# Performance work log

Measured on AMD Instinct MI355X. Metric: run time of the kernel, lower is better.

Reference implementation:

```python
import jax, jax.numpy as jnp
import numpy as np

B, N, M, D = 256, 256, 256, 4
BIG = 1e10  # stand-in for +inf that keeps grads of unselected branches finite


def chamfer_split(target, reco, in_pid, out_pid):
    # masks of 'real' (non-zero pid) particles
    mask_x = in_pid != 0          # [B, N]
    mask_y = out_pid != 0         # [B, M]
    nx = jnp.sum(mask_x, axis=-1)  # [B] actual counts
    ny = jnp.sum(mask_y, axis=-1)
    n_in = jnp.maximum(1, nx).astype(target.dtype)   # max(1, n_in_part)
    n_out = jnp.maximum(1, ny).astype(target.dtype)  # max(1, n_out_part)

    # pairwise euclidean distances [B, N, M]
    diff = target[:, :, None, :] - reco[:, None, :, :]   # [B, N, M, D]
    dist = jnp.sqrt(jnp.sum(diff * diff, axis=-1))       # [B, N, M]

    # masked dual-axis mins (invalid entries pushed to BIG)
    min_xy = jnp.min(jnp.where(mask_y[:, None, :], dist, BIG), axis=-1)  # [B, N]
    min_yx = jnp.min(jnp.where(mask_x[:, :, None], dist, BIG), axis=-2)  # [B, M]
    sum_xy = jnp.sum(jnp.where(mask_x, min_xy, 0.0), axis=-1)  # [B]
    sum_yx = jnp.sum(jnp.where(mask_y, min_yx, 0.0), axis=-1)  # [B]

    normal = 0.5 * (sum_xy / n_out + sum_yx / n_in)  # [B]

    # edge cases: no reco non-zero particles -> sum||x_nz|| / max(1,nx);
    # no target non-zero particles -> sum over empty set = 0
    norm_x = jnp.linalg.norm(target, axis=-1)                    # [B, N]
    sum_norm_x_nz = jnp.sum(jnp.where(mask_x, norm_x, 0.0), -1)  # [B]
    eucl_non_zero = jnp.where(ny == 0, sum_norm_x_nz / n_in,
                              jnp.where(nx == 0, jnp.zeros_like(normal), normal))

    # zero-pid reco particles: mean L2 norm over zero entries
    norm_y = jnp.linalg.norm(reco, axis=-1)                          # [B, M]
    sum_norm_y_zero = jnp.sum(jnp.where(~mask_y, norm_y, 0.0), -1)   # [B]
    n_zero = jnp.maximum(1, reco.shape[1] - ny).astype(reco.dtype)
    eucl_zero = sum_norm_y_zero / n_zero

    # reduction == 'mean'
    return jnp.mean(eucl_non_zero), jnp.mean(eucl_zero)


def setup_inputs() -> dict:
    key = jax.random.key(0)
    k1, k2, k3, k4 = jax.random.split(key, 4)
    target = jax.random.normal(k1, (B, N, D), dtype=jnp.float32)
    reco = jax.random.normal(k2, (B, M, D), dtype=jnp.float32)
    in_pid = jax.random.randint(k3, (B, N), 0, 5, dtype=jnp.int32)
    out_pid = jax.random.randint(k4, (B, M), 0, 5, dtype=jnp.int32)
    return {"target": target, "reco": reco, "in_pid": in_pid, "out_pid": out_pid}


def reference(target, reco, in_pid, out_pid):
    return chamfer_split(target, reco, in_pid, out_pid)
```

## Files before the change

kernel.cpp:

```cpp
#include <hip/hip_runtime.h>
#include <math.h>

#define BB 256
#define NN 256
#define MM 256

#define POISON  1.0e18f
#define MINSENT 3.0e38f

__global__ __launch_bounds__(1024) void chamfer_split_kernel(
    const float* __restrict__ target,
    const float* __restrict__ reco,
    const int*   __restrict__ in_pid,
    const int*   __restrict__ out_pid,
    float* __restrict__ out)
{
    const int b = blockIdx.x;
    const int t = threadIdx.x;

    __shared__ float4 sT[NN];
    __shared__ float4 sR[MM];
    __shared__ float  pmin1[4][NN];
    __shared__ float  pmin2[4][MM];
    __shared__ int    sNx, sNy;
    __shared__ float  wsum[4][4];

    float4 x = {0.f, 0.f, 0.f, 0.f};
    float4 y = {0.f, 0.f, 0.f, 0.f};
    int mx = 0, my = 0;
    if (t == 0) { sNx = 0; sNy = 0; }
    if (t < NN) {
        const float4* tg = (const float4*)(target + (size_t)b * NN * 4);
        const float4* rc = (const float4*)(reco   + (size_t)b * MM * 4);
        x = tg[t];
        y = rc[t];
        mx = (in_pid[b * NN + t] != 0);
        my = (out_pid[b * MM + t] != 0);
        float4 px = x, py = y;
        if (!mx) px = make_float4(POISON, POISON, POISON, POISON);
        if (!my) py = make_float4(POISON, POISON, POISON, POISON);
        sT[t] = px;
        sR[t] = py;
        unsigned long long bx = __ballot(mx);
        unsigned long long by = __ballot(my);
        if ((t & 63) == 0) {
            atomicAdd(&sNx, (int)__popcll(bx));
            atomicAdd(&sNy, (int)__popcll(by));
        }
    }
    __syncthreads();

    if (t < 512) {
        const int c  = t >> 7;
        const int n0 = t & 127;
        const float4 xa = sT[n0];
        const float4 xb = sT[n0 + 128];
        float ma = MINSENT, mb = MINSENT;
        const int mbase = c << 6;
        #pragma unroll 16
        for (int i = 0; i < 64; ++i) {
            const float4 r = sR[mbase + i];
            float d0 = xa.x - r.x, d1 = xa.y - r.y, d2 = xa.z - r.z, d3 = xa.w - r.w;
            float sa = fmaf(d0, d0, fmaf(d1, d1, fmaf(d2, d2, d3 * d3)));
            ma = fminf(ma, sa);
            d0 = xb.x - r.x; d1 = xb.y - r.y; d2 = xb.z - r.z; d3 = xb.w - r.w;
            float sb = fmaf(d0, d0, fmaf(d1, d1, fmaf(d2, d2, d3 * d3)));
            mb = fminf(mb, sb);
        }
        pmin1[c][n0]       = ma;
        pmin1[c][n0 + 128] = mb;
    } else {
        const int u  = t - 512;
        const int c  = u >> 7;
        const int m0 = u & 127;
        const float4 ya = sR[m0];
        const float4 yb = sR[m0 + 128];
        float ma = MINSENT, mb = MINSENT;
        const int nbase = c << 6;
        #pragma unroll 16
        for (int i = 0; i < 64; ++i) {
            const float4 p = sT[nbase + i];
            float d0 = p.x - ya.x, d1 = p.y - ya.y, d2 = p.z - ya.z, d3 = p.w - ya.w;
            float sa = fmaf(d0, d0, fmaf(d1, d1, fmaf(d2, d2, d3 * d3)));
            ma = fminf(ma, sa);
            d0 = p.x - yb.x; d1 = p.y - yb.y; d2 = p.z - yb.z; d3 = p.w - yb.w;
            float sb = fmaf(d0, d0, fmaf(d1, d1, fmaf(d2, d2, d3 * d3)));
            mb = fminf(mb, sb);
        }
        pmin2[c][m0]       = ma;
        pmin2[c][m0 + 128] = mb;
    }
    __syncthreads();

    float v_xy = 0.f, v_yx = 0.f, v_nx = 0.f, v_ny0 = 0.f;
    if (t < NN) {
        const float mxy = fminf(fminf(pmin1[0][t], pmin1[1][t]),
                                fminf(pmin1[2][t], pmin1[3][t]));
        const float myx = fminf(fminf(pmin2[0][t], pmin2[1][t]),
                                fminf(pmin2[2][t], pmin2[3][t]));
        v_xy = mx ? sqrtf(mxy) : 0.f;
        v_yx = my ? sqrtf(myx) : 0.f;
        const float normx = sqrtf(fmaf(x.x, x.x, fmaf(x.y, x.y, fmaf(x.z, x.z, x.w * x.w))));
        const float normy = sqrtf(fmaf(y.x, y.x, fmaf(y.y, y.y, fmaf(y.z, y.z, y.w * y.w))));
        v_nx  = mx ? normx : 0.f;
        v_ny0 = my ? 0.f : normy;

        #pragma unroll
        for (int off = 32; off > 0; off >>= 1) {
            v_xy  += __shfl_down(v_xy,  off, 64);
            v_yx  += __shfl_down(v_yx,  off, 64);
            v_nx  += __shfl_down(v_nx,  off, 64);
            v_ny0 += __shfl_down(v_ny0, off, 64);
        }
        if ((t & 63) == 0) {
            const int wave = t >> 6;
            wsum[wave][0] = v_xy;
            wsum[wave][1] = v_yx;
            wsum[wave][2] = v_nx;
            wsum[wave][3] = v_ny0;
        }
    }
    __syncthreads();

    if (t == 0) {
        float s_xy = 0.f, s_yx = 0.f, s_nx = 0.f, s_ny0 = 0.f;
        #pragma unroll
        for (int w = 0; w < 4; ++w) {
            s_xy  += wsum[w][0];
            s_yx  += wsum[w][1];
            s_nx  += wsum[w][2];
            s_ny0 += wsum[w][3];
        }
        const int   nx    = sNx;
        const int   ny    = sNy;
        const float n_in  = (float)max(1, nx);
        const float n_out = (float)max(1, ny);
        const float normal = 0.5f * (s_xy / n_out + s_yx / n_in);
        const float eucl_nz = (ny == 0) ? (s_nx / n_in)
                                        : ((nx == 0) ? 0.0f : normal);
        const float n_zero = (float)max(1, MM - ny);
        const float eucl_z = s_ny0 / n_zero;
        atomicAdd(&out[0], eucl_nz * (1.0f / BB));
        atomicAdd(&out[1], eucl_z  * (1.0f / BB));
    }
}

extern "C" void kernel_launch(void* const* d_in, const int* in_sizes, int n_in,
                              void* d_out, int out_size, void* d_ws, size_t ws_size,
                              hipStream_t stream) {
    const float* target  = (const float*)d_in[0];
    const float* reco    = (const float*)d_in[1];
    const int*   in_pid  = (const int*)d_in[2];
    const int*   out_pid = (const int*)d_in[3];
    float* out = (float*)d_out;

    hipMemsetAsync(out, 0, (size_t)out_size * sizeof(float), stream);

    chamfer_split_kernel<<<dim3(BB), dim3(1024), 0, stream>>>(
        target, reco, in_pid, out_pid, out);
}
```

Baseline: 74.61 us.

## Register-block 8 points per thread and replace atomics with a two-stage reduction

Each thread now keeps 8 own-side points in registers and scans a 16-element chunk of the other side. Every shared-memory load of the other point is therefore reused 8 times instead of 2, cutting LDS traffic per distance. The partial-min buffers grow to 16 chunks, which adds LDS footprint and a longer final min. The global atomics and the memset are replaced by a per-batch workspace write plus a small second kernel, trading one memset launch for one extra kernel launch with a deterministic sum.

```diff
diff --git a/kernel.cpp b/kernel.cpp
--- a/kernel.cpp
+++ b/kernel.cpp
@@ -8,27 +8,26 @@
 #define POISON  1.0e18f
 #define MINSENT 3.0e38f
 
-__global__ __launch_bounds__(1024) void chamfer_split_kernel(
+__global__ __launch_bounds__(1024) void chamfer_batch_kernel(
     const float* __restrict__ target,
     const float* __restrict__ reco,
     const int*   __restrict__ in_pid,
     const int*   __restrict__ out_pid,
-    float* __restrict__ out)
+    float2* __restrict__ ws)
 {
     const int b = blockIdx.x;
     const int t = threadIdx.x;
 
     __shared__ float4 sT[NN];
     __shared__ float4 sR[MM];
-    __shared__ float  pmin1[4][NN];
-    __shared__ float  pmin2[4][MM];
-    __shared__ int    sNx, sNy;
+    __shared__ float  pmin1[16][NN];
+    __shared__ float  pmin2[16][MM];
+    __shared__ int    sCx[4], sCy[4];
     __shared__ float  wsum[4][4];
 
     float4 x = {0.f, 0.f, 0.f, 0.f};
     float4 y = {0.f, 0.f, 0.f, 0.f};
     int mx = 0, my = 0;
-    if (t == 0) { sNx = 0; sNy = 0; }
     if (t < NN) {
         const float4* tg = (const float4*)(target + (size_t)b * NN * 4);
         const float4* rc = (const float4*)(reco   + (size_t)b * MM * 4);
@@ -44,60 +43,73 @@
         unsigned long long bx = __ballot(mx);
         unsigned long long by = __ballot(my);
         if ((t & 63) == 0) {
-            atomicAdd(&sNx, (int)__popcll(bx));
-            atomicAdd(&sNy, (int)__popcll(by));
+            sCx[t >> 6] = (int)__popcll(bx);
+            sCy[t >> 6] = (int)__popcll(by);
         }
     }
     __syncthreads();
 
-    if (t < 512) {
-        const int c  = t >> 7;
-        const int n0 = t & 127;
-        const float4 xa = sT[n0];
-        const float4 xb = sT[n0 + 128];
-        float ma = MINSENT, mb = MINSENT;
-        const int mbase = c << 6;
-        #pragma unroll 16
-        for (int i = 0; i < 64; ++i) {
-            const float4 r = sR[mbase + i];
-            float d0 = xa.x - r.x, d1 = xa.y - r.y, d2 = xa.z - r.z, d3 = xa.w - r.w;
-            float sa = fmaf(d0, d0, fmaf(d1, d1, fmaf(d2, d2, d3 * d3)));
-            ma = fminf(ma, sa);
-            d0 = xb.x - r.x; d1 = xb.y - r.y; d2 = xb.z - r.z; d3 = xb.w - r.w;
-            float sb = fmaf(d0, d0, fmaf(d1, d1, fmaf(d2, d2, d3 * d3)));
-            mb = fminf(mb, sb);
+    {
+        const bool pass1 = (t < 512);
+        const int  u = pass1 ? t : (t - 512);
+        const int  c = u >> 5;
+        const int  g = u & 31;
+        const float4* own   = pass1 ? sT : sR;
+        const float4* other = pass1 ? sR : sT;
+        float (*pout)[256]  = pass1 ? pmin1 : pmin2;
+
+        float4 p0 = own[g];
+        float4 p1 = own[g + 32];
+        float4 p2 = own[g + 64];
+        float4 p3 = own[g + 96];
+        float4 p4 = own[g + 128];
+        float4 p5 = own[g + 160];
+        float4 p6 = own[g + 192];
+        float4 p7 = own[g + 224];
+        float m0 = MINSENT, m1 = MINSENT, m2 = MINSENT, m3 = MINSENT;
+        float m4 = MINSENT, m5 = MINSENT, m6 = MINSENT, m7 = MINSENT;
+        const int base = c << 4;
+        #pragma unroll 4
+        for (int i = 0; i < 16; ++i) {
+            const float4 r = other[base + i];
+            float d0, d1, d2, d3, sq;
+            d0 = p0.x - r.x; d1 = p0.y - r.y; d2 = p0.z - r.z; d3 = p0.w - r.w;
+            sq = fmaf(d0, d0, fmaf(d1, d1, fmaf(d2, d2, d3 * d3))); m0 = fminf(m0, sq);
+            d0 = p1.x - r.x; d1 = p1.y - r.y; d2 = p1.z - r.z; d3 = p1.w - r.w;
+            sq = fmaf(d0, d0, fmaf(d1, d1, fmaf(d2, d2, d3 * d3))); m1 = fminf(m1, sq);
+            d0 = p2.x - r.x; d1 = p2.y - r.y; d2 = p2.z - r.z; d3 = p2.w - r.w;
+            sq = fmaf(d0, d0, fmaf(d1, d1, fmaf(d2, d2, d3 * d3))); m2 = fminf(m2, sq);
+            d0 = p3.x - r.x; d1 = p3.y - r.y; d2 = p3.z - r.z; d3 = p3.w - r.w;
+            sq = fmaf(d0, d0, fmaf(d1, d1, fmaf(d2, d2, d3 * d3))); m3 = fminf(m3, sq);
+            d0 = p4.x - r.x; d1 = p4.y - r.y; d2 = p4.z - r.z; d3 = p4.w - r.w;
+            sq = fmaf(d0, d0, fmaf(d1, d1, fmaf(d2, d2, d3 * d3))); m4 = fminf(m4, sq);
+            d0 = p5.x - r.x; d1 = p5.y - r.y; d2 = p5.z - r.z; d3 = p5.w - r.w;
+            sq = fmaf(d0, d0, fmaf(d1, d1, fmaf(d2, d2, d3 * d3))); m5 = fminf(m5, sq);
+            d0 = p6.x - r.x; d1 = p6.y - r.y; d2 = p6.z - r.z; d3 = p6.w - r.w;
+            sq = fmaf(d0, d0, fmaf(d1, d1, fmaf(d2, d2, d3 * d3))); m6 = fminf(m6, sq);
+            d0 = p7.x - r.x; d1 = p7.y - r.y; d2 = p7.z - r.z; d3 = p7.w - r.w;
+            sq = fmaf(d0, d0, fmaf(d1, d1, fmaf(d2, d2, d3 * d3))); m7 = fminf(m7, sq);
         }
-        pmin1[c][n0]       = ma;
-        pmin1[c][n0 + 128] = mb;
-    } else {
-        const int u  = t - 512;
-        const int c  = u >> 7;
-        const int m0 = u & 127;
-        const float4 ya = sR[m0];
-        const float4 yb = sR[m0 + 128];
-        float ma = MINSENT, mb = MINSENT;
-        const int nbase = c << 6;
-        #pragma unroll 16
-        for (int i = 0; i < 64; ++i) {
-            const float4 p = sT[nbase + i];
-            float d0 = p.x - ya.x, d1 = p.y - ya.y, d2 = p.z - ya.z, d3 = p.w - ya.w;
-            float sa = fmaf(d0, d0, fmaf(d1, d1, fmaf(d2, d2, d3 * d3)));
-            ma = fminf(ma, sa);
-            d0 = p.x - yb.x; d1 = p.y - yb.y; d2 = p.z - yb.z; d3 = p.w - yb.w;
-            float sb = fmaf(d0, d0, fmaf(d1, d1, fmaf(d2, d2, d3 * d3)));
-            mb = fminf(mb, sb);
-        }
-        pmin2[c][m0]       = ma;
-        pmin2[c][m0 + 128] = mb;
+        pout[c][g]       = m0;
+        pout[c][g + 32]  = m1;
+        pout[c][g + 64]  = m2;
+        pout[c][g + 96]  = m3;
+        pout[c][g + 128] = m4;
+        pout[c][g + 160] = m5;
+        pout[c][g + 192] = m6;
+        pout[c][g + 224] = m7;
     }
     __syncthreads();
 
     float v_xy = 0.f, v_yx = 0.f, v_nx = 0.f, v_ny0 = 0.f;
     if (t < NN) {
-        const float mxy = fminf(fminf(pmin1[0][t], pmin1[1][t]),
-                                fminf(pmin1[2][t], pmin1[3][t]));
-        const float myx = fminf(fminf(pmin2[0][t], pmin2[1][t]),
-                                fminf(pmin2[2][t], pmin2[3][t]));
+        float mxy = pmin1[0][t];
+        float myx = pmin2[0][t];
+        #pragma unroll
+        for (int c = 1; c < 16; ++c) {
+            mxy = fminf(mxy, pmin1[c][t]);
+            myx = fminf(myx, pmin2[c][t]);
+        }
         v_xy = mx ? sqrtf(mxy) : 0.f;
         v_yx = my ? sqrtf(myx) : 0.f;
         const float normx = sqrtf(fmaf(x.x, x.x, fmaf(x.y, x.y, fmaf(x.z, x.z, x.w * x.w))));
@@ -124,15 +136,16 @@
 
     if (t == 0) {
         float s_xy = 0.f, s_yx = 0.f, s_nx = 0.f, s_ny0 = 0.f;
+        int nx = 0, ny = 0;
         #pragma unroll
         for (int w = 0; w < 4; ++w) {
             s_xy  += wsum[w][0];
             s_yx  += wsum[w][1];
             s_nx  += wsum[w][2];
             s_ny0 += wsum[w][3];
+            nx    += sCx[w];
+            ny    += sCy[w];
         }
-        const int   nx    = sNx;
-        const int   ny    = sNy;
         const float n_in  = (float)max(1, nx);
         const float n_out = (float)max(1, ny);
         const float normal = 0.5f * (s_xy / n_out + s_yx / n_in);
@@ -140,8 +153,29 @@
                                         : ((nx == 0) ? 0.0f : normal);
         const float n_zero = (float)max(1, MM - ny);
         const float eucl_z = s_ny0 / n_zero;
-        atomicAdd(&out[0], eucl_nz * (1.0f / BB));
-        atomicAdd(&out[1], eucl_z  * (1.0f / BB));
+        ws[b] = make_float2(eucl_nz, eucl_z);
+    }
+}
+
+__global__ __launch_bounds__(256) void chamfer_final_kernel(
+    const float2* __restrict__ ws, float* __restrict__ out)
+{
+    const int t = threadIdx.x;
+    __shared__ float2 s[4];
+    float2 v = ws[t];
+    #pragma unroll
+    for (int off = 32; off > 0; off >>= 1) {
+        v.x += __shfl_down(v.x, off, 64);
+        v.y += __shfl_down(v.y, off, 64);
+    }
+    if ((t & 63) == 0) s[t >> 6] = v;
+    __syncthreads();
+    if (t == 0) {
+        float a = 0.f, bsum = 0.f;
+        #pragma unroll
+        for (int w = 0; w < 4; ++w) { a += s[w].x; bsum += s[w].y; }
+        out[0] = a * (1.0f / BB);
+        out[1] = bsum * (1.0f / BB);
     }
 }
 
@@ -153,9 +187,9 @@
     const int*   in_pid  = (const int*)d_in[2];
     const int*   out_pid = (const int*)d_in[3];
     float* out = (float*)d_out;
+    float2* ws = (float2*)d_ws;
 
-    hipMemsetAsync(out, 0, (size_t)out_size * sizeof(float), stream);
-
-    chamfer_split_kernel<<<dim3(BB), dim3(1024), 0, stream>>>(
-        target, reco, in_pid, out_pid, out);
+    chamfer_batch_kernel<<<dim3(BB), dim3(1024), 0, stream>>>(
+        target, reco, in_pid, out_pid, ws);
+    chamfer_final_kernel<<<dim3(1), dim3(256), 0, stream>>>(ws, out);
 }
```

Measured after the change: 68.10 us. 8.7% less time.
